# Kernel optimization log

Hardware: AMD Instinct MI355X
Metric: run time of the kernel (lower is better)

The kernel has to match this reference:

```python
import math
import jax, jax.numpy as jnp
import numpy as np

D_MODEL = 512
D_STATE = 256
BATCH = 16
SEQ = 2048


def setup_inputs() -> dict:
    key = jax.random.key(0)
    k_x, k_len, k_bre, k_bim, k_cre, k_cim = jax.random.split(key, 6)
    scale_b = 1.0 / math.sqrt(D_MODEL)
    scale_c = 1.0 / math.sqrt(D_STATE)
    return {
        "x": jax.random.normal(k_x, (BATCH, SEQ, D_MODEL), dtype=jnp.float32),
        "lengths": jax.random.randint(k_len, (BATCH,), 0, SEQ).astype(jnp.int64),
        "lambda_real_log": jnp.log(jnp.linspace(0.5, 1.5, D_STATE, dtype=jnp.float32)),
        "lambda_imag": jnp.linspace(0.0, math.pi, D_STATE, dtype=jnp.float32),
        "log_dt": jnp.asarray(-2.0, dtype=jnp.float32),
        "B_re": jax.random.normal(k_bre, (D_STATE, D_MODEL), dtype=jnp.float32) * scale_b,
        "B_im": jax.random.normal(k_bim, (D_STATE, D_MODEL), dtype=jnp.float32) * scale_b,
        "C_re": jax.random.normal(k_cre, (D_MODEL, D_STATE), dtype=jnp.float32) * scale_c,
        "C_im": jax.random.normal(k_cim, (D_MODEL, D_STATE), dtype=jnp.float32) * scale_c,
        "D_weight": jnp.eye(D_MODEL, dtype=jnp.float32),
    }


def reference(x, lengths, lambda_real_log, lambda_imag, log_dt, B_re, B_im, C_re, C_im, D_weight):
    B, L, _ = x.shape
    # Discretization (ZOH on diagonal complex lambda)
    dt = jax.nn.softplus(log_dt) + 0.0001
    lam = -jnp.exp(lambda_real_log) + 1j * lambda_imag          # [N] complex
    abar = jnp.exp(dt * lam)                                    # [N]
    b = B_re + 1j * B_im                                        # [N, D]
    c = C_re + 1j * C_im                                        # [D, N]
    bbar = ((abar - 1.0) / lam)[:, None] * b                    # [N, D]

    # Precompute input terms for all steps: u_t @ bbar^T -> [B, L, N] complex
    xc = x.astype(jnp.complex64)
    input_terms = jnp.einsum("bld,nd->bln", xc, bbar)

    valid = jnp.arange(L)[:, None] < lengths[None, :]           # [L, B] bool

    def step(state, inp):
        it, v = inp                                             # it: [B,N], v: [B]
        new_state = jnp.where(v[:, None], state * abar[None, :] + it, state)
        return new_state, new_state

    init = jnp.zeros((B, D_STATE), dtype=jnp.complex64)
    _, states = jax.lax.scan(step, init, (input_terms.transpose(1, 0, 2), valid))  # [L, B, N]

    response = jnp.einsum("lbn,dn->bld", states, c).real        # [B, L, D]
    y = response + x @ D_weight.T

    mask = (jnp.arange(L)[None, :] < lengths[:, None])[:, :, None]
    return y * mask.astype(y.dtype)
```

## Files before the change

### kernel.cpp

```cpp
#include <hip/hip_runtime.h>
#include <hip/hip_bf16.h>
#include <stdint.h>

#define D_MODEL 512
#define D_STATE 256
#define BATCH   16
#define SEQ     2048
#define M_ROWS  (BATCH*SEQ)
#define JN      512
#define BM      32
#define NCHUNK  (SEQ/BM)
#define TM      64

#define OFF_W1    0u
#define OFF_W2    (512u*512u*2u)
#define OFF_ABAR  (1048576u)
#define OFF_ABARC (OFF_ABAR + 2048u)
#define OFF_U     (2097152u)
#define OFF_CARRY (OFF_U + (unsigned)M_ROWS*256u*4u)
#define OFF_FIN   (OFF_CARRY + 2097152u)
#define WS_NEED_SPLIT (OFF_FIN + 2097152u)

typedef __bf16 bf16x8 __attribute__((ext_vector_type(8)));
typedef float  f32x4  __attribute__((ext_vector_type(4)));

__device__ __forceinline__ unsigned short f2bf(float f) {
  unsigned int u = __float_as_uint(f);
  u += 0x7fffu + ((u >> 16) & 1u);
  return (unsigned short)(u >> 16);
}
__device__ __forceinline__ float bf2f(unsigned int h) { return __uint_as_float(h << 16); }
__device__ __forceinline__ float2 cmul(float2 a, float2 b) {
  return make_float2(a.x*b.x - a.y*b.y, a.x*b.y + a.y*b.x);
}

__global__ __launch_bounds__(256) void prep(const float* __restrict__ lrl, const float* __restrict__ lim,
                                            const float* __restrict__ ldt,
                                            const float* __restrict__ Bre, const float* __restrict__ Bim,
                                            const float* __restrict__ Cre, const float* __restrict__ Cim,
                                            char* __restrict__ ws) {
  int f = blockIdx.x * 256 + threadIdx.x;
  float dt = log1pf(expf(ldt[0])) + 1e-4f;

  int fr = f & 32767;
  int w  = fr >> 12, ks = (fr >> 8) & 15, cf = (fr >> 6) & 3, l = fr & 63;
  int lan = l & 15;
  int kb  = ks * 32 + (l >> 4) * 8;

  unsigned int out[4];
  if (f < 32768) {
    int j = (cf >> 1) * 256 + w * 32 + (cf & 1) * 16 + lan;
    int n = j & 255;
    float lre = -expf(lrl[n]);
    float li  = lim[n];
    float er  = expf(dt * lre);
    float are = er * cosf(dt * li);
    float aim = er * sinf(dt * li);
    float nre = are - 1.0f, nim = aim;
    float den = lre*lre + li*li;
    float cre = (nre*lre + nim*li) / den;
    float cim = (nim*lre - nre*li) / den;
    bool isIm = (j >= 256);
    #pragma unroll
    for (int p = 0; p < 4; ++p) {
      unsigned short e0, e1;
      #pragma unroll
      for (int q = 0; q < 2; ++q) {
        int d = kb + p * 2 + q;
        float br = Bre[n*512 + d], bi = Bim[n*512 + d];
        float v = isIm ? (cre*bi + cim*br) : (cre*br - cim*bi);
        if (q == 0) e0 = f2bf(v); else e1 = f2bf(v);
      }
      out[p] = (unsigned int)e0 | ((unsigned int)e1 << 16);
    }
    *(uint4*)(ws + OFF_W1 + (size_t)fr * 16) = make_uint4(out[0], out[1], out[2], out[3]);
  } else {
    int j = w * 64 + cf * 16 + lan;
    #pragma unroll
    for (int p = 0; p < 4; ++p) {
      unsigned short e0, e1;
      #pragma unroll
      for (int q = 0; q < 2; ++q) {
        int k = kb + p * 2 + q;
        int n2 = k >> 1;
        float v = (k & 1) ? -Cim[j*256 + n2] : Cre[j*256 + n2];
        if (q == 0) e0 = f2bf(v); else e1 = f2bf(v);
      }
      out[p] = (unsigned int)e0 | ((unsigned int)e1 << 16);
    }
    *(uint4*)(ws + OFF_W2 + (size_t)fr * 16) = make_uint4(out[0], out[1], out[2], out[3]);
  }

  if (f < 256) {
    int nn = f;
    float lre2 = -expf(lrl[nn]);
    float li2  = lim[nn];
    float er2  = expf(dt * lre2);
    float2* A  = (float2*)(ws + OFF_ABAR);
    float2* AC = (float2*)(ws + OFF_ABARC);
    A[nn]  = make_float2(er2 * cosf(dt * li2), er2 * sinf(dt * li2));
    float erC = expf((float)BM * dt * lre2);
    float thC = (float)BM * dt * li2;
    AC[nn] = make_float2(erC * cosf(thC), erC * sinf(thC));
  }
}

__global__ __launch_bounds__(512, 4) void gemm1(const float* __restrict__ x,
                                                char* __restrict__ ws,
                                                float2* __restrict__ FIN) {
  __shared__ __align__(16) char buf[64 * 1024];
  int blk = blockIdx.x;
  int m0 = blk * TM;
  int tid = threadIdx.x;
  const bf16x8* W1f = (const bf16x8*)(ws + OFF_W1);
  unsigned int* U = (unsigned int*)(ws + OFF_U);

  const float4* xv = (const float4*)(x + (size_t)m0 * 512);
  #pragma unroll 16
  for (int it = 0; it < 16; ++it) {
    int i = it * 512 + tid;
    float4 v = xv[i];
    int e = i * 4; int row = e >> 9; int col = e & 511;
    unsigned int lo = (unsigned int)f2bf(v.x) | ((unsigned int)f2bf(v.y) << 16);
    unsigned int hi = (unsigned int)f2bf(v.z) | ((unsigned int)f2bf(v.w) << 16);
    int byte = ((row * JN + col) * 2) ^ ((row & 7) << 4);
    *(uint2*)(buf + byte) = make_uint2(lo, hi);
  }
  __syncthreads();

  int w = tid >> 6, l = tid & 63;
  int lan = l & 15, kg = (l >> 4) * 8;

  f32x4 acc[4][4];
  #pragma unroll
  for (int i = 0; i < 4; ++i)
    #pragma unroll
    for (int jj = 0; jj < 4; ++jj) acc[i][jj] = (f32x4){0.f, 0.f, 0.f, 0.f};

  size_t wbase = (size_t)(w * 16) * 4 * 64 + l;
  bf16x8 bpre[4];
  #pragma unroll
  for (int cf = 0; cf < 4; ++cf) bpre[cf] = W1f[wbase + (size_t)cf * 64];

  __builtin_amdgcn_s_setprio(1);
  for (int ks = 0; ks < 16; ++ks) {
    int kb = ks * 32 + kg;
    bf16x8 bcur[4];
    #pragma unroll
    for (int cf = 0; cf < 4; ++cf) bcur[cf] = bpre[cf];
    if (ks < 15) {
      #pragma unroll
      for (int cf = 0; cf < 4; ++cf) bpre[cf] = W1f[wbase + (size_t)((ks + 1) * 4 + cf) * 64];
    }
    bf16x8 afr[4];
    #pragma unroll
    for (int rf = 0; rf < 4; ++rf) {
      int row = rf * 16 + lan;
      int byte = ((row * JN + kb) * 2) ^ ((row & 7) << 4);
      afr[rf] = *(const bf16x8*)(buf + byte);
    }
    #pragma unroll
    for (int cf = 0; cf < 4; ++cf)
      #pragma unroll
      for (int rf = 0; rf < 4; ++rf)
        acc[rf][cf] = __builtin_amdgcn_mfma_f32_16x16x32_bf16(afr[rf], bcur[cf], acc[rf][cf], 0, 0, 0);
  }
  __builtin_amdgcn_s_setprio(0);

  __syncthreads();
  #pragma unroll
  for (int rf = 0; rf < 4; ++rf) {
    #pragma unroll
    for (int cf = 0; cf < 2; ++cf) {
      int n = w * 32 + cf * 16 + lan;
      #pragma unroll
      for (int rr = 0; rr < 4; ++rr) {
        int r = rf * 16 + (l >> 4) * 4 + rr;
        unsigned int pk = (unsigned int)f2bf(acc[rf][cf][rr]) |
                          ((unsigned int)f2bf(acc[rf][cf + 2][rr]) << 16);
        int byte = (r * 1024 + n * 4) ^ ((r & 7) << 4);
        *(unsigned int*)(buf + byte) = pk;
      }
    }
  }
  __syncthreads();

  {
    int ch = tid >> 8;
    int n = tid & 255;
    float2 a = ((const float2*)(ws + OFF_ABAR))[n];
    float sre = 0.f, sim = 0.f;
    unsigned int* Up = U + (size_t)(m0 + ch * BM) * 256 + n;
    #pragma unroll 8
    for (int t = 0; t < BM; ++t) {
      int r = ch * BM + t;
      unsigned int uv = *(const unsigned int*)(buf + ((r * 1024 + n * 4) ^ ((r & 7) << 4)));
      float nr = fmaf(sre, a.x, fmaf(-sim, a.y, bf2f(uv & 0xffffu)));
      float ni = fmaf(sre, a.y, fmaf( sim, a.x, bf2f(uv >> 16)));
      sre = nr; sim = ni;
      Up[(size_t)t * 256] = (unsigned int)f2bf(sre) | ((unsigned int)f2bf(sim) << 16);
    }
    FIN[(size_t)(blk * 2 + ch) * 256 + n] = make_float2(sre, sim);
  }
}

__global__ __launch_bounds__(256) void scanB(const float2* __restrict__ FIN,
                                             float2* __restrict__ CI,
                                             char* __restrict__ ws) {
  int b = blockIdx.x;
  int n = threadIdx.x;
  const float2* AC = (const float2*)(ws + OFF_ABARC);
  float2 ac = AC[n];
  float cre = 0.f, cim = 0.f;
  #pragma unroll 8
  for (int k = 0; k < NCHUNK; ++k) {
    size_t idx = (size_t)(b * NCHUNK + k) * 256 + n;
    float2 fin = FIN[idx];
    CI[idx] = make_float2(cre, cim);
    float nr = fmaf(cre, ac.x, fmaf(-cim, ac.y, fin.x));
    float ni = fmaf(cre, ac.y, fmaf( cim, ac.x, fin.y));
    cre = nr; cim = ni;
  }
}

__global__ __launch_bounds__(512, 4) void corr_gemm2(const float* __restrict__ x,
                                                     const int* __restrict__ lengths,
                                                     float* __restrict__ y,
                                                     char* __restrict__ ws,
                                                     const float2* __restrict__ CI) {
  __shared__ __align__(16) char smem[64 * 1024];
  int blk = blockIdx.x;
  int b = blk >> 5;
  int seq0 = (blk & 31) * TM;
  int m0 = blk * TM;
  int tid = threadIdx.x;
  int w = tid >> 6, l = tid & 63;

  {
    const float2* A = (const float2*)(ws + OFF_ABAR);
    const uint4* Uv = (const uint4*)((const unsigned int*)(ws + OFF_U) + (size_t)m0 * 256);
    float2 ap[4], a8[4], c0[4], c1[4], e[4];
    #pragma unroll
    for (int q = 0; q < 4; ++q) {
      float2 a1 = A[4*l + q];
      float2 a2 = cmul(a1, a1);
      float2 a4 = cmul(a2, a2);
      a8[q] = cmul(a4, a4);
      int wp = w + 1;
      float2 t = make_float2(1.f, 0.f);
      if (wp & 1) t = a1;
      if (wp & 2) t = cmul(t, a2);
      if (wp & 4) t = cmul(t, a4);
      if (wp & 8) t = cmul(t, a8[q]);
      ap[q] = t;
      c0[q] = CI[(size_t)(blk * 2    ) * 256 + 4*l + q];
      c1[q] = CI[(size_t)(blk * 2 + 1) * 256 + 4*l + q];
    }
    #pragma unroll
    for (int i = 0; i < 8; ++i) {
      int t = w + 8 * i;
      if (i == 0) {
        for (int q = 0; q < 4; ++q) e[q] = cmul(c0[q], ap[q]);
      }
      if (i == 4) {
        for (int q = 0; q < 4; ++q) e[q] = cmul(c1[q], ap[q]);
      }
      uint4 sv = Uv[(size_t)t * 64 + l];
      unsigned int out[4];
      #pragma unroll
      for (int q = 0; q < 4; ++q) {
        unsigned int u = (q == 0) ? sv.x : (q == 1) ? sv.y : (q == 2) ? sv.z : sv.w;
        float sr = bf2f(u & 0xffffu) + e[q].x;
        float si = bf2f(u >> 16)     + e[q].y;
        out[q] = (unsigned int)f2bf(sr) | ((unsigned int)f2bf(si) << 16);
        e[q] = cmul(e[q], a8[q]);
      }
      int byte = (t * 1024 + l * 16) ^ ((t & 7) << 4);
      *(uint4*)(smem + byte) = make_uint4(out[0], out[1], out[2], out[3]);
    }
  }
  __syncthreads();

  const bf16x8* W2f = (const bf16x8*)(ws + OFF_W2);
  int lan = l & 15, kg = (l >> 4) * 8;

  f32x4 acc[4][4];
  #pragma unroll
  for (int i = 0; i < 4; ++i)
    #pragma unroll
    for (int jj = 0; jj < 4; ++jj) acc[i][jj] = (f32x4){0.f, 0.f, 0.f, 0.f};

  size_t wbase = (size_t)(w * 16) * 4 * 64 + l;
  bf16x8 bpre[4];
  #pragma unroll
  for (int cf = 0; cf < 4; ++cf) bpre[cf] = W2f[wbase + (size_t)cf * 64];

  __builtin_amdgcn_s_setprio(1);
  for (int ks = 0; ks < 16; ++ks) {
    int kb = ks * 32 + kg;
    bf16x8 bcur[4];
    #pragma unroll
    for (int cf = 0; cf < 4; ++cf) bcur[cf] = bpre[cf];
    if (ks < 15) {
      #pragma unroll
      for (int cf = 0; cf < 4; ++cf) bpre[cf] = W2f[wbase + (size_t)((ks + 1) * 4 + cf) * 64];
    }
    bf16x8 aS[4];
    #pragma unroll
    for (int rf = 0; rf < 4; ++rf) {
      int row = rf * 16 + lan;
      int byte = ((row * JN + kb) * 2) ^ ((row & 7) << 4);
      aS[rf] = *(const bf16x8*)(smem + byte);
    }
    #pragma unroll
    for (int cf = 0; cf < 4; ++cf)
      #pragma unroll
      for (int rf = 0; rf < 4; ++rf)
        acc[rf][cf] = __builtin_amdgcn_mfma_f32_16x16x32_bf16(aS[rf], bcur[cf], acc[rf][cf], 0, 0, 0);
  }
  __builtin_amdgcn_s_setprio(0);

  int len = lengths[b];
  #pragma unroll
  for (int pass = 0; pass < 2; ++pass) {
    __syncthreads();
    #pragma unroll
    for (int rf2 = 0; rf2 < 2; ++rf2) {
      int rf = pass * 2 + rf2;
      #pragma unroll
      for (int cf = 0; cf < 4; ++cf) {
        int col = w * 64 + cf * 16 + lan;
        #pragma unroll
        for (int rr = 0; rr < 4; ++rr) {
          int r = rf2 * 16 + (l >> 4) * 4 + rr;
          int byte = (r * 2048 + col * 4) ^ ((r & 7) << 4);
          *(float*)(smem + byte) = acc[rf][cf][rr];
        }
      }
    }
    __syncthreads();
    #pragma unroll
    for (int it = 0; it < 8; ++it) {
      int f = it * 512 + tid;
      int r = f >> 7, c4 = f & 127;
      int byte = (r * 2048 + c4 * 16) ^ ((r & 7) << 4);
      f32x4 v = *(const f32x4*)(smem + byte);
      int row = pass * 32 + r;
      int m = m0 + row;
      int lseq = seq0 + row;
      const f32x4 xv = *(const f32x4*)(x + (size_t)m * 512 + c4 * 4);
      f32x4 outv;
      if (lseq < len) {
        outv[0] = v[0] + xv[0]; outv[1] = v[1] + xv[1];
        outv[2] = v[2] + xv[2]; outv[3] = v[3] + xv[3];
      } else {
        outv = (f32x4){0.f, 0.f, 0.f, 0.f};
      }
      *(f32x4*)(y + (size_t)m * 512 + c4 * 4) = outv;
    }
  }
}

extern "C" void kernel_launch(void* const* d_in, const int* in_sizes, int n_in,
                              void* d_out, int out_size, void* d_ws, size_t ws_size,
                              hipStream_t stream) {
  const float* x       = (const float*)d_in[0];
  const int*   lengths = (const int*)d_in[1];
  const float* lrl     = (const float*)d_in[2];
  const float* lim     = (const float*)d_in[3];
  const float* ldt     = (const float*)d_in[4];
  const float* Bre     = (const float*)d_in[5];
  const float* Bim     = (const float*)d_in[6];
  const float* Cre     = (const float*)d_in[7];
  const float* Cim     = (const float*)d_in[8];
  float* y = (float*)d_out;
  char*  ws = (char*)d_ws;

  float2* carry = (float2*)(ws + OFF_CARRY);
  float2* fin   = (ws_size >= (size_t)WS_NEED_SPLIT) ? (float2*)(ws + OFF_FIN) : carry;

  prep<<<256, 256, 0, stream>>>(lrl, lim, ldt, Bre, Bim, Cre, Cim, ws);
  gemm1<<<M_ROWS / TM, 512, 0, stream>>>(x, ws, fin);
  scanB<<<BATCH, 256, 0, stream>>>(fin, carry, ws);
  corr_gemm2<<<M_ROWS / TM, 512, 0, stream>>>(x, lengths, y, ws, carry);
}
```

Baseline: 74.97 us.

## Skip sequence tiles beyond each batch length and interleave tile order

```diff
diff --git a/kernel.cpp b/kernel.cpp
--- a/kernel.cpp
+++ b/kernel.cpp
@@ -11,6 +11,7 @@
 #define BM      32
 #define NCHUNK  (SEQ/BM)
 #define TM      64
+#define NTILE   (M_ROWS/TM)
 
 #define OFF_W1    0u
 #define OFF_W2    (512u*512u*2u)
@@ -32,6 +33,9 @@
 __device__ __forceinline__ float bf2f(unsigned int h) { return __uint_as_float(h << 16); }
 __device__ __forceinline__ float2 cmul(float2 a, float2 b) {
   return make_float2(a.x*b.x - a.y*b.y, a.x*b.y + a.y*b.x);
+}
+__device__ __forceinline__ int tile_remap(int phys) {
+  return (phys & 1) ? (NTILE - 1 - (phys >> 1)) : (phys >> 1);
 }
 
 __global__ __launch_bounds__(256) void prep(const float* __restrict__ lrl, const float* __restrict__ lim,
@@ -106,11 +110,15 @@
 }
 
 __global__ __launch_bounds__(512, 4) void gemm1(const float* __restrict__ x,
+                                                const int* __restrict__ lengths,
                                                 char* __restrict__ ws,
                                                 float2* __restrict__ FIN) {
   __shared__ __align__(16) char buf[64 * 1024];
-  int blk = blockIdx.x;
-  int m0 = blk * TM;
+  int tile = tile_remap(blockIdx.x);
+  int bat = tile >> 5;
+  int sp  = (tile & 31) * TM;
+  if (lengths[bat] <= sp) return;
+  int m0 = tile * TM;
   int tid = threadIdx.x;
   const bf16x8* W1f = (const bf16x8*)(ws + OFF_W1);
   unsigned int* U = (unsigned int*)(ws + OFF_U);
@@ -200,7 +208,7 @@
       sre = nr; sim = ni;
       Up[(size_t)t * 256] = (unsigned int)f2bf(sre) | ((unsigned int)f2bf(sim) << 16);
     }
-    FIN[(size_t)(blk * 2 + ch) * 256 + n] = make_float2(sre, sim);
+    FIN[(size_t)(tile * 2 + ch) * 256 + n] = make_float2(sre, sim);
   }
 }
 
@@ -229,11 +237,21 @@
                                                      char* __restrict__ ws,
                                                      const float2* __restrict__ CI) {
   __shared__ __align__(16) char smem[64 * 1024];
-  int blk = blockIdx.x;
-  int b = blk >> 5;
-  int seq0 = (blk & 31) * TM;
-  int m0 = blk * TM;
+  int tile = tile_remap(blockIdx.x);
+  int b = tile >> 5;
+  int seq0 = (tile & 31) * TM;
+  int m0 = tile * TM;
   int tid = threadIdx.x;
+  int len = lengths[b];
+
+  if (len <= seq0) {
+    f32x4* yp = (f32x4*)(y + (size_t)m0 * 512);
+    f32x4 z = (f32x4){0.f, 0.f, 0.f, 0.f};
+    #pragma unroll 16
+    for (int it = 0; it < 16; ++it) yp[it * 512 + tid] = z;
+    return;
+  }
+
   int w = tid >> 6, l = tid & 63;
 
   {
@@ -253,8 +271,8 @@
       if (wp & 4) t = cmul(t, a4);
       if (wp & 8) t = cmul(t, a8[q]);
       ap[q] = t;
-      c0[q] = CI[(size_t)(blk * 2    ) * 256 + 4*l + q];
-      c1[q] = CI[(size_t)(blk * 2 + 1) * 256 + 4*l + q];
+      c0[q] = CI[(size_t)(tile * 2    ) * 256 + 4*l + q];
+      c1[q] = CI[(size_t)(tile * 2 + 1) * 256 + 4*l + q];
     }
     #pragma unroll
     for (int i = 0; i < 8; ++i) {
@@ -320,7 +338,6 @@
   }
   __builtin_amdgcn_s_setprio(0);
 
-  int len = lengths[b];
   #pragma unroll
   for (int pass = 0; pass < 2; ++pass) {
     __syncthreads();
@@ -380,7 +397,7 @@
   float2* fin   = (ws_size >= (size_t)WS_NEED_SPLIT) ? (float2*)(ws + OFF_FIN) : carry;
 
   prep<<<256, 256, 0, stream>>>(lrl, lim, ldt, Bre, Bim, Cre, Cim, ws);
-  gemm1<<<M_ROWS / TM, 512, 0, stream>>>(x, ws, fin);
+  gemm1<<<NTILE, 512, 0, stream>>>(x, lengths, ws, fin);
   scanB<<<BATCH, 256, 0, stream>>>(fin, carry, ws);
-  corr_gemm2<<<M_ROWS / TM, 512, 0, stream>>>(x, lengths, y, ws, carry);
-}
+  corr_gemm2<<<NTILE, 512, 0, stream>>>(x, lengths, y, ws, carry);
+}
```

After: 64.73 us (median of 2 runs). 13.7% less time.
